# Kernel tuning notes

Measured on AMD Instinct MI355X. Metric: run time of the kernel, lower is better.

The kernel has to match this reference:

```python
import jax, jax.numpy as jnp
import numpy as np

N_NODES = 50000
N_EDGES = 600000
NFEAT = 256
NHID = 128
NCLASS = 40


def setup_inputs() -> dict:
    key = jax.random.key(0)
    ks = jax.random.split(key, 10)
    x = jax.random.normal(ks[0], (N_NODES, NFEAT), dtype=jnp.float32)
    edge_src = jax.random.randint(ks[1], (N_EDGES,), 0, N_NODES, dtype=jnp.int32)
    edge_dst = jax.random.randint(ks[2], (N_EDGES,), 0, N_NODES, dtype=jnp.int32)
    # normalized adjacency weights (positive, ~1/deg scale)
    edge_weight = jax.random.uniform(ks[3], (N_EDGES,), dtype=jnp.float32) * 0.2
    # GraphConvolution params (Glorot-ish init)
    W1 = jax.random.normal(ks[4], (NFEAT, NHID), dtype=jnp.float32) / np.float32(np.sqrt(NFEAT))
    b1 = jnp.zeros((NHID,), dtype=jnp.float32)
    W2 = jax.random.normal(ks[5], (NHID, NHID), dtype=jnp.float32) / np.float32(np.sqrt(NHID))
    b2 = jnp.zeros((NHID,), dtype=jnp.float32)
    W3 = jax.random.normal(ks[6], (NHID, NCLASS), dtype=jnp.float32) / np.float32(np.sqrt(NHID))
    b3 = jnp.zeros((NCLASS,), dtype=jnp.float32)
    return {"x": x, "edge_weight": edge_weight, "W1": W1, "b1": b1,
            "W2": W2, "b2": b2, "W3": W3, "b3": b3,
            "edge_src": edge_src, "edge_dst": edge_dst}


def _gcn_layer(h, W, b, edge_src, edge_dst, edge_weight):
    # support = h @ W ; out = spmm(adj, support) + b
    support = h @ W                                   # [N, out]
    msgs = support[edge_src] * edge_weight[:, None]   # [E, out]
    agg = jax.ops.segment_sum(msgs, edge_dst, num_segments=N_NODES)
    return agg + b


def reference(x, edge_weight, W1, b1, W2, b2, W3, b3, edge_src, edge_dst):
    # eval mode: F.dropout(training=False) is identity
    h = jax.nn.relu(_gcn_layer(x, W1, b1, edge_src, edge_dst, edge_weight))
    h = jax.nn.relu(_gcn_layer(h, W2, b2, edge_src, edge_dst, edge_weight))
    h = _gcn_layer(h, W3, b3, edge_src, edge_dst, edge_weight)
    return jax.nn.log_softmax(h, axis=1)
```

## Files before the change

### kernel.cpp

```cpp
#include <hip/hip_runtime.h>
#include <math.h>

#define N_NODES 50000
#define N_EDGES 600000
#define NFEAT   256
#define NHID    128
#define NCLASS  40
#define NBUCK 196
#define EPB_A 2048
#define BUCK_CAP 4096
#define BUCK_WIN 5888
#define BINA_BLOCKS ((N_EDGES + EPB_A - 1) / EPB_A)
#define CVTW_BLOCKS 224
#define GEMM_BLOCKS ((N_NODES + 63) / 64)

typedef __attribute__((ext_vector_type(8))) short bf16x8;
typedef __attribute__((ext_vector_type(4))) float f32x4;
typedef __attribute__((ext_vector_type(2))) float f32x2;

__device__ inline ushort f2bf(float f) {
    uint u = __float_as_uint(f);
    uint r = (u + 0x7fffu + ((u >> 16) & 1u)) >> 16;
    return (ushort)r;
}

__global__ __launch_bounds__(256) void binA_cvtw(const int* __restrict__ src,
                                                 const int* __restrict__ dst,
                                                 const float* __restrict__ w,
                                                 int* __restrict__ bucket_cnt,
                                                 int2* __restrict__ staging, int E,
                                                 const float* __restrict__ W1,
                                                 const float* __restrict__ W2,
                                                 const float* __restrict__ W3,
                                                 ushort* __restrict__ BT1,
                                                 ushort* __restrict__ BT2,
                                                 ushort* __restrict__ BT3) {
    int tid = threadIdx.x;
    if ((int)blockIdx.x >= BINA_BLOCKS) {
        int idx = ((int)blockIdx.x - BINA_BLOCKS) * 256 + tid;
        if (idx < 32768) {
            int nr = idx >> 8, k = idx & 255;
            BT1[idx] = f2bf(W1[(size_t)k * 128 + nr]);
        } else if (idx < 49152) {
            int t = idx - 32768;
            int nr = t >> 7, k = t & 127;
            BT2[t] = f2bf(W2[(size_t)k * 128 + nr]);
        } else if (idx < 57344) {
            int t = idx - 49152;
            int nr = t >> 7, k = t & 127;
            BT3[t] = (nr < 40) ? f2bf(W3[(size_t)k * 40 + nr]) : (ushort)0;
        }
        return;
    }
    __shared__ int lh[NBUCK];
    for (int b = tid; b < NBUCK; b += 256) lh[b] = 0;
    __syncthreads();
    int base = blockIdx.x * EPB_A;
    int d[8];
    #pragma unroll
    for (int j = 0; j < 8; ++j) {
        int i = base + j * 256 + tid;
        d[j] = (i < E) ? dst[i] : -1;
        if (d[j] >= 0) atomicAdd(&lh[d[j] >> 8], 1);
    }
    __syncthreads();
    for (int b = tid; b < NBUCK; b += 256) {
        int c = lh[b];
        lh[b] = c ? (b * BUCK_CAP + atomicAdd(&bucket_cnt[b], c)) : 0;
    }
    __syncthreads();
    #pragma unroll
    for (int j = 0; j < 8; ++j) {
        int i = base + j * 256 + tid;
        if (d[j] >= 0) {
            int slot = atomicAdd(&lh[d[j] >> 8], 1);
            uint rec = ((uint)f2bf(w[i]) << 16) | (uint)src[i];
            staging[slot] = make_int2((int)rec, d[j] & 255);
        }
    }
}

template<int NT, bool AF32>
__device__ __forceinline__ void gemm_body(const void* __restrict__ Ain,
                                          const ushort* __restrict__ BT,
                                          int M, int K, int Nout,
                                          ushort* __restrict__ Cout, int row0) {
    __shared__ ushort a_s[64 * 40];
    __shared__ ushort b_s[64 * NT * 40];
    int tid = threadIdx.x;
    int wave = tid >> 6, lane = tid & 63;
    int lr = lane & 15, lk = (lane >> 4) * 8;
    f32x4 acc[4][NT];
    #pragma unroll
    for (int mt = 0; mt < 4; ++mt)
        #pragma unroll
        for (int nt = 0; nt < NT; ++nt) acc[mt][nt] = (f32x4){0.f, 0.f, 0.f, 0.f};

    for (int k0 = 0; k0 < K; k0 += 32) {
        {
            int r = tid >> 2, c8 = (tid & 3) * 8;
            int gr = row0 + r; if (gr >= M) gr = M - 1;
            if (AF32) {
                const float* Af = (const float*)Ain;
                float4 v0 = *(const float4*)(Af + (size_t)gr * K + k0 + c8);
                float4 v1 = *(const float4*)(Af + (size_t)gr * K + k0 + c8 + 4);
                ushort4 o0, o1;
                o0.x = f2bf(v0.x); o0.y = f2bf(v0.y); o0.z = f2bf(v0.z); o0.w = f2bf(v0.w);
                o1.x = f2bf(v1.x); o1.y = f2bf(v1.y); o1.z = f2bf(v1.z); o1.w = f2bf(v1.w);
                *(ushort4*)(a_s + r * 40 + c8) = o0;
                *(ushort4*)(a_s + r * 40 + c8 + 4) = o1;
            } else {
                const ushort* Ab = (const ushort*)Ain;
                float4 v = *(const float4*)(Ab + (size_t)gr * K + k0 + c8);
                *(float4*)(a_s + r * 40 + c8) = v;
            }
        }
        #pragma unroll
        for (int i = 0; i < NT; ++i) {
            int idx = tid * NT + i;
            int r = idx >> 2, c8 = (idx & 3) * 8;
            float4 v = *(const float4*)(BT + (size_t)r * K + k0 + c8);
            *(float4*)(b_s + r * 40 + c8) = v;
        }
        __syncthreads();
        bf16x8 bfr[NT];
        #pragma unroll
        for (int nt = 0; nt < NT; ++nt)
            bfr[nt] = *(const bf16x8*)(b_s + ((wave * NT + nt) * 16 + lr) * 40 + lk);
        #pragma unroll
        for (int mt = 0; mt < 4; ++mt) {
            bf16x8 afr = *(const bf16x8*)(a_s + (mt * 16 + lr) * 40 + lk);
            #pragma unroll
            for (int nt = 0; nt < NT; ++nt)
                acc[mt][nt] = __builtin_amdgcn_mfma_f32_16x16x32_bf16(
                    afr, bfr[nt], acc[mt][nt], 0, 0, 0);
        }
        __syncthreads();
    }
    int col0 = wave * NT * 16;
    #pragma unroll
    for (int mt = 0; mt < 4; ++mt) {
        int gr0 = row0 + mt * 16 + (lane >> 4) * 4;
        #pragma unroll
        for (int nt = 0; nt < NT; ++nt) {
            int gc = col0 + nt * 16 + lr;
            #pragma unroll
            for (int i = 0; i < 4; ++i) {
                int gr = gr0 + i;
                if (gr < M && gc < Nout)
                    Cout[(size_t)gr * Nout + gc] = f2bf(acc[mt][nt][i]);
            }
        }
    }
}

__global__ __launch_bounds__(256) void scan_gemm1(const int* __restrict__ bucket_cnt,
                                                  const int2* __restrict__ staging,
                                                  int2* __restrict__ rsp2,
                                                  uint* __restrict__ edges,
                                                  const float* __restrict__ x,
                                                  const ushort* __restrict__ BT1,
                                                  ushort* __restrict__ supA) {
    if ((int)blockIdx.x >= NBUCK) {
        gemm_body<2, true>(x, BT1, N_NODES, 256, 128, supA,
                           ((int)blockIdx.x - NBUCK) * 64);
        return;
    }
    __shared__ int hist[256];
    __shared__ int buf[256];
    __shared__ int lcur[256];
    int tid = threadIdx.x;
    hist[tid] = 0;
    __syncthreads();
    int b = blockIdx.x;
    int c = bucket_cnt[b];
    const int2* st = staging + (size_t)b * BUCK_CAP;
    for (int p = tid; p < c; p += 256) atomicAdd(&hist[st[p].y], 1);
    __syncthreads();
    int v = (hist[tid] + 7) & ~7;
    buf[tid] = v;
    __syncthreads();
    #pragma unroll
    for (int off = 1; off < 256; off <<= 1) {
        int t = (tid >= off) ? buf[tid - off] : 0;
        __syncthreads();
        buf[tid] += t;
        __syncthreads();
    }
    int bb = b * BUCK_WIN;
    int ex = buf[tid] - v + bb;
    int i = b * 256 + tid;
    if (i < N_NODES) rsp2[i] = make_int2(ex, ex + v);
    lcur[tid] = ex;
    __syncthreads();
    int e0 = bb + buf[255];
    for (int p = bb + tid; p < e0; p += 256) edges[p] = 0;
    __syncthreads();
    for (int p = tid; p < c; p += 256) {
        int2 r = st[p];
        int slot = atomicAdd(&lcur[r.y], 1);
        edges[slot] = (uint)r.x;
    }
}


#define LDREC(Ra, Rb, Rc, Rd, POS) do { \
    const uint4* _p = (const uint4*)(edges + (POS)); \
    Ra = _p[0]; Rb = _p[1]; Rc = _p[2]; Rd = _p[3]; \
} while (0)

#define GATHER(P, W, Ra, Rb, Rc, Rd) do { \
    uint _r[16] = {Ra.x, Ra.y, Ra.z, Ra.w, Rb.x, Rb.y, Rb.z, Rb.w, \
                   Rc.x, Rc.y, Rc.z, Rc.w, Rd.x, Rd.y, Rd.z, Rd.w}; \
    _Pragma("unroll") \
    for (int _j = 0; _j < 16; ++_j) { \
        uint _idx = _r[_j] & 0xffffu; \
        if (_idx >= N_NODES) _idx = N_NODES - 1;   \
        P[_j] = sup[(size_t)_idx * 64 + lane]; \
        W[_j] = __uint_as_float(_r[_j] & 0xffff0000u); \
    } \
} while (0)

#define FLUSH1() do { \
    uint _pk = ((uint)f2bf(fmaxf(acc2.y + by, 0.f)) << 16) \
             |  (uint)f2bf(fmaxf(acc2.x + bx, 0.f)); \
    *(uint*)(&a4_s[ks][(wave * 16 + cur) * 40 + kk]) = _pk; \
    acc2 = (f32x2){0.f, 0.f}; \
    ++cur; \
    e_cur = (cur < 16) ? e_s[wave][cur + 1] : 0x7fffffff; \
} while (0)

#define FMA_CHUNK(QB, P, W) do { \
    _Pragma("unroll") \
    for (int _g = 0; _g < 2; ++_g) { \
        int _qg = (QB) + _g * 8; \
        while (cur < 16 && _qg >= e_cur) FLUSH1(); \
        if (_qg < QE) { \
            _Pragma("unroll") \
            for (int _j = 0; _j < 8; ++_j) { \
                uint _pv = P[_g * 8 + _j]; \
                f32x2 _v; \
                _v.x = __uint_as_float(_pv << 16); \
                _v.y = __uint_as_float(_pv & 0xffff0000u); \
                float _w = W[_g * 8 + _j]; \
                acc2 += _v * (f32x2){_w, _w}; \
            } \
        } \
    } \
} while (0)

template<int NT>
__device__ __forceinline__ void fused_body(const uint* __restrict__ sup,
                                           const int2* __restrict__ rsp2,
                                           const uint* __restrict__ edges,
                                           const float* __restrict__ bias,
                                           const ushort* __restrict__ BT,
                                           int Nout,
                                           ushort* __restrict__ Cout) {
    __shared__ ushort a4_s[4][64 * 40];
    __shared__ int e_s[4][17];
    int tid = threadIdx.x;
    int wave = tid >> 6, lane = tid & 63;
    int row0 = blockIdx.x * 64;
    int nfirst = row0 + wave * 16;
    float bx = bias[2 * lane], by = bias[2 * lane + 1];
    int ks = lane >> 4;
    int kk = 2 * (lane & 15);

    if (lane < 16) {
        int nd = nfirst + lane; if (nd >= N_NODES) nd = N_NODES - 1;
        int2 t = rsp2[nd];
        e_s[wave][lane + 1] = t.y;
        if (lane == 0) e_s[wave][0] = t.x;
    }
    __syncthreads();
    int Q = e_s[wave][0], QE = e_s[wave][16];
    int cur = 0, e_cur = e_s[wave][1];
    f32x2 acc2 = (f32x2){0.f, 0.f};

    uint4 rA0, rA1, rA2, rA3, rB0, rB1, rB2, rB3;
    uint pa[16], pb[16];
    float wa[16], wb[16];
    int q = Q;
    LDREC(rA0, rA1, rA2, rA3, q);
    GATHER(pa, wa, rA0, rA1, rA2, rA3);
    LDREC(rB0, rB1, rB2, rB3, q + 16);
    while (q < QE) {
        GATHER(pb, wb, rB0, rB1, rB2, rB3);
        LDREC(rA0, rA1, rA2, rA3, q + 32);
        FMA_CHUNK(q, pa, wa);
        q += 16;
        if (q >= QE) break;
        GATHER(pa, wa, rA0, rA1, rA2, rA3);
        LDREC(rB0, rB1, rB2, rB3, q + 32);
        FMA_CHUNK(q, pb, wb);
        q += 16;
    }
    while (cur < 16) FLUSH1();
    __syncthreads();

    int lr = lane & 15, lk = (lane >> 4) * 8;
    f32x4 acc[4][NT];
    #pragma unroll
    for (int mt = 0; mt < 4; ++mt)
        #pragma unroll
        for (int nt = 0; nt < NT; ++nt) acc[mt][nt] = (f32x4){0.f, 0.f, 0.f, 0.f};
    #pragma unroll
    for (int ksi = 0; ksi < 4; ++ksi) {
        int k0 = ksi * 32;
        bf16x8 bfr[NT];
        #pragma unroll
        for (int nt = 0; nt < NT; ++nt)
            bfr[nt] = *(const bf16x8*)(BT +
                (size_t)((wave * NT + nt) * 16 + lr) * 128 + k0 + lk);
        #pragma unroll
        for (int mt = 0; mt < 4; ++mt) {
            bf16x8 afr = *(const bf16x8*)(&a4_s[ksi][(mt * 16 + lr) * 40 + lk]);
            #pragma unroll
            for (int nt = 0; nt < NT; ++nt)
                acc[mt][nt] = __builtin_amdgcn_mfma_f32_16x16x32_bf16(
                    afr, bfr[nt], acc[mt][nt], 0, 0, 0);
        }
    }
    int col0 = wave * NT * 16;
    #pragma unroll
    for (int mt = 0; mt < 4; ++mt) {
        int gr0 = row0 + mt * 16 + (lane >> 4) * 4;
        #pragma unroll
        for (int nt = 0; nt < NT; ++nt) {
            int gc = col0 + nt * 16 + lr;
            #pragma unroll
            for (int i = 0; i < 4; ++i) {
                int gr = gr0 + i;
                if (gr < N_NODES && gc < Nout)
                    Cout[(size_t)gr * Nout + gc] = f2bf(acc[mt][nt][i]);
            }
        }
    }
}

__global__ __launch_bounds__(256) void fused_ag2(const uint* __restrict__ sup,
                                                 const int2* __restrict__ rsp2,
                                                 const uint* __restrict__ edges,
                                                 const float* __restrict__ bias,
                                                 const ushort* __restrict__ BT,
                                                 ushort* __restrict__ Cout) {
    fused_body<2>(sup, rsp2, edges, bias, BT, 128, Cout);
}

__global__ __launch_bounds__(256) void fused_ag3(const uint* __restrict__ sup,
                                                 const int2* __restrict__ rsp2,
                                                 const uint* __restrict__ edges,
                                                 const float* __restrict__ bias,
                                                 const ushort* __restrict__ BT,
                                                 ushort* __restrict__ Cout) {
    fused_body<1>(sup, rsp2, edges, bias, BT, 40, Cout);
}

__global__ __launch_bounds__(256) void spmm40_lsm(const ushort* __restrict__ sup,
                                                  const int2* __restrict__ rsp2,
                                                  const uint* __restrict__ edges,
                                                  const float* __restrict__ bias,
                                                  float* __restrict__ out, int n) {
    int wid = blockIdx.x * 4 + (threadIdx.x >> 6);
    int lane = threadIdx.x & 63;
    if (wid >= n) return;
    int2 ke = rsp2[wid];
    int k = ke.x, e = ke.y;
    float acc = 0.f;
    int lf = (lane < 40) ? lane : 39;
    if (k < e) {
        const uint4* q4 = (const uint4*)(edges + k);
        uint4 qa = q4[0], qb = q4[1];
        for (; k < e; k += 8) {
            int kn = k + 8;
            int kc = (kn < e) ? kn : k;
            const uint4* n4 = (const uint4*)(edges + kc);
            uint4 na = n4[0], nb4 = n4[1];
            uint q[8] = {qa.x, qa.y, qa.z, qa.w, qb.x, qb.y, qb.z, qb.w};
            float p[8];
            #pragma unroll
            for (int j = 0; j < 8; ++j) {
                uint us = sup[(size_t)(q[j] & 0xffffu) * 40 + lf];
                p[j] = __uint_as_float(us << 16);
            }
            #pragma unroll
            for (int j = 0; j < 8; ++j)
                acc += p[j] * __uint_as_float(q[j] & 0xffff0000u);
            qa = na; qb = nb4;
        }
    }
    float v = (lane < 40) ? acc + bias[lane] : -INFINITY;
    float m = v;
    #pragma unroll
    for (int off = 32; off; off >>= 1) m = fmaxf(m, __shfl_xor(m, off, 64));
    float ex = (lane < 40) ? expf(v - m) : 0.f;
    float s = ex;
    #pragma unroll
    for (int off = 32; off; off >>= 1) s += __shfl_xor(s, off, 64);
    float ls = logf(s);
    if (lane < 40) out[(size_t)wid * 40 + lane] = v - m - ls;
}

extern "C" void kernel_launch(void* const* d_in, const int* in_sizes, int n_in,
                              void* d_out, int out_size, void* d_ws, size_t ws_size,
                              hipStream_t stream) {
    const float* x   = (const float*)d_in[0];
    const float* ew  = (const float*)d_in[1];
    const float* W1  = (const float*)d_in[2];
    const float* b1  = (const float*)d_in[3];
    const float* W2  = (const float*)d_in[4];
    const float* b2  = (const float*)d_in[5];
    const float* W3  = (const float*)d_in[6];
    const float* b3  = (const float*)d_in[7];
    const int* esrc  = (const int*)d_in[8];
    const int* edst  = (const int*)d_in[9];
    float* out = (float*)d_out;

    char* ws = (char*)d_ws;
    size_t off = 0;
    auto alloc = [&](size_t bytes) {
        size_t cur = off;
        off += (bytes + 255) & ~(size_t)255;
        return cur;
    };
    int* bucket_cnt = (int*)(ws + alloc(256 * sizeof(int)));
    int2* rsp2   = (int2*)(ws + alloc((size_t)N_NODES * sizeof(int2)));
    uint* edges  = (uint*)(ws + alloc((size_t)NBUCK * BUCK_WIN * sizeof(uint)));
    int2* staging = (int2*)(ws + alloc((size_t)NBUCK * BUCK_CAP * sizeof(int2)));
    ushort* BT1  = (ushort*)(ws + alloc(128 * 256 * 2));
    ushort* BT2  = (ushort*)(ws + alloc(128 * 128 * 2));
    ushort* BT3  = (ushort*)(ws + alloc(64 * 128 * 2));
    char* Sreg   = ws + alloc((size_t)N_NODES * 128 * 2);
    char* Hreg   = ws + alloc((size_t)N_NODES * 128 * 2);
    (void)alloc((size_t)66000 * 128 * 2);

    ushort* supA = (ushort*)Sreg;
    ushort* supB = (ushort*)Hreg;
    ushort* sup3 = (ushort*)Sreg;

    hipMemsetAsync(bucket_cnt, 0, 256 * sizeof(int), stream);
    binA_cvtw<<<BINA_BLOCKS + CVTW_BLOCKS, 256, 0, stream>>>(
        esrc, edst, ew, bucket_cnt, staging, N_EDGES, W1, W2, W3, BT1, BT2, BT3);
    scan_gemm1<<<NBUCK + GEMM_BLOCKS, 256, 0, stream>>>(
        bucket_cnt, staging, rsp2, edges, x, BT1, supA);
    fused_ag2<<<GEMM_BLOCKS, 256, 0, stream>>>(
        (const uint*)supA, rsp2, edges, b1, BT2, supB);
    fused_ag3<<<GEMM_BLOCKS, 256, 0, stream>>>(
        (const uint*)supB, rsp2, edges, b2, BT3, sup3);
    spmm40_lsm<<<(N_NODES + 3) / 4, 256, 0, stream>>>(sup3, rsp2, edges, b3,
                                                      out, N_NODES);
}
```

Baseline: 216.2 us.

## Halve fused aggregation tile to 32 rows and use segmented final aggregation with log-softmax

The fused aggregate+GEMM kernels now process 32 nodes per block (8 per wave), which doubles the block count and shrinks shared memory. The third-layer support is stored with a 64-column padded stride so the final layer can reuse the prefetched, segmented edge-walk pattern. The old one-wave-per-node spmm40_lsm kernel is replaced by agg_lsm, which streams edges across 8 nodes per wave and runs log-softmax at each node boundary. The trade-offs are more per-block setup and less MFMA reuse per B-fragment load, plus a wider sup3 write with 24 wasted columns.

Result: no change. 215.4 us (-0.4%).

```diff
diff --git a/kernel.cpp b/kernel.cpp
--- a/kernel.cpp
+++ b/kernel.cpp
@@ -13,6 +13,7 @@
 #define BINA_BLOCKS ((N_EDGES + EPB_A - 1) / EPB_A)
 #define CVTW_BLOCKS 224
 #define GEMM_BLOCKS ((N_NODES + 63) / 64)
+#define TILE_BLOCKS ((N_NODES + 31) / 32)
 
 typedef __attribute__((ext_vector_type(8))) short bf16x8;
 typedef __attribute__((ext_vector_type(4))) float f32x4;
@@ -221,20 +222,20 @@
     } \
 } while (0)
 
-#define FLUSH1() do { \
+#define FLUSH_A() do { \
     uint _pk = ((uint)f2bf(fmaxf(acc2.y + by, 0.f)) << 16) \
              |  (uint)f2bf(fmaxf(acc2.x + bx, 0.f)); \
-    *(uint*)(&a4_s[ks][(wave * 16 + cur) * 40 + kk]) = _pk; \
+    *(uint*)(&a4_s[ks][(wave * 8 + cur) * 40 + kk]) = _pk; \
     acc2 = (f32x2){0.f, 0.f}; \
     ++cur; \
-    e_cur = (cur < 16) ? e_s[wave][cur + 1] : 0x7fffffff; \
-} while (0)
-
-#define FMA_CHUNK(QB, P, W) do { \
+    e_cur = (cur < 8) ? e_s[wave][cur + 1] : 0x7fffffff; \
+} while (0)
+
+#define FMA_CHUNK_A(QB, P, W) do { \
     _Pragma("unroll") \
     for (int _g = 0; _g < 2; ++_g) { \
         int _qg = (QB) + _g * 8; \
-        while (cur < 16 && _qg >= e_cur) FLUSH1(); \
+        while (cur < 8 && _qg >= e_cur) FLUSH_A(); \
         if (_qg < QE) { \
             _Pragma("unroll") \
             for (int _j = 0; _j < 8; ++_j) { \
@@ -257,24 +258,24 @@
                                            const ushort* __restrict__ BT,
                                            int Nout,
                                            ushort* __restrict__ Cout) {
-    __shared__ ushort a4_s[4][64 * 40];
-    __shared__ int e_s[4][17];
+    __shared__ ushort a4_s[4][32 * 40];
+    __shared__ int e_s[4][9];
     int tid = threadIdx.x;
     int wave = tid >> 6, lane = tid & 63;
-    int row0 = blockIdx.x * 64;
-    int nfirst = row0 + wave * 16;
+    int row0 = blockIdx.x * 32;
+    int nfirst = row0 + wave * 8;
     float bx = bias[2 * lane], by = bias[2 * lane + 1];
     int ks = lane >> 4;
     int kk = 2 * (lane & 15);
 
-    if (lane < 16) {
+    if (lane < 8) {
         int nd = nfirst + lane; if (nd >= N_NODES) nd = N_NODES - 1;
         int2 t = rsp2[nd];
         e_s[wave][lane + 1] = t.y;
         if (lane == 0) e_s[wave][0] = t.x;
     }
     __syncthreads();
-    int Q = e_s[wave][0], QE = e_s[wave][16];
+    int Q = e_s[wave][0], QE = e_s[wave][8];
     int cur = 0, e_cur = e_s[wave][1];
     f32x2 acc2 = (f32x2){0.f, 0.f};
 
@@ -288,21 +289,21 @@
     while (q < QE) {
         GATHER(pb, wb, rB0, rB1, rB2, rB3);
         LDREC(rA0, rA1, rA2, rA3, q + 32);
-        FMA_CHUNK(q, pa, wa);
+        FMA_CHUNK_A(q, pa, wa);
         q += 16;
         if (q >= QE) break;
         GATHER(pa, wa, rA0, rA1, rA2, rA3);
         LDREC(rB0, rB1, rB2, rB3, q + 32);
-        FMA_CHUNK(q, pb, wb);
+        FMA_CHUNK_A(q, pb, wb);
         q += 16;
     }
-    while (cur < 16) FLUSH1();
+    while (cur < 8) FLUSH_A();
     __syncthreads();
 
     int lr = lane & 15, lk = (lane >> 4) * 8;
-    f32x4 acc[4][NT];
-    #pragma unroll
-    for (int mt = 0; mt < 4; ++mt)
+    f32x4 acc[2][NT];
+    #pragma unroll
+    for (int mt = 0; mt < 2; ++mt)
         #pragma unroll
         for (int nt = 0; nt < NT; ++nt) acc[mt][nt] = (f32x4){0.f, 0.f, 0.f, 0.f};
     #pragma unroll
@@ -314,7 +315,7 @@
             bfr[nt] = *(const bf16x8*)(BT +
                 (size_t)((wave * NT + nt) * 16 + lr) * 128 + k0 + lk);
         #pragma unroll
-        for (int mt = 0; mt < 4; ++mt) {
+        for (int mt = 0; mt < 2; ++mt) {
             bf16x8 afr = *(const bf16x8*)(&a4_s[ksi][(mt * 16 + lr) * 40 + lk]);
             #pragma unroll
             for (int nt = 0; nt < NT; ++nt)
@@ -324,7 +325,7 @@
     }
     int col0 = wave * NT * 16;
     #pragma unroll
-    for (int mt = 0; mt < 4; ++mt) {
+    for (int mt = 0; mt < 2; ++mt) {
         int gr0 = row0 + mt * 16 + (lane >> 4) * 4;
         #pragma unroll
         for (int nt = 0; nt < NT; ++nt) {
@@ -354,52 +355,93 @@
                                                  const float* __restrict__ bias,
                                                  const ushort* __restrict__ BT,
                                                  ushort* __restrict__ Cout) {
-    fused_body<1>(sup, rsp2, edges, bias, BT, 40, Cout);
-}
-
-__global__ __launch_bounds__(256) void spmm40_lsm(const ushort* __restrict__ sup,
-                                                  const int2* __restrict__ rsp2,
-                                                  const uint* __restrict__ edges,
-                                                  const float* __restrict__ bias,
-                                                  float* __restrict__ out, int n) {
-    int wid = blockIdx.x * 4 + (threadIdx.x >> 6);
-    int lane = threadIdx.x & 63;
-    if (wid >= n) return;
-    int2 ke = rsp2[wid];
-    int k = ke.x, e = ke.y;
-    float acc = 0.f;
-    int lf = (lane < 40) ? lane : 39;
-    if (k < e) {
-        const uint4* q4 = (const uint4*)(edges + k);
-        uint4 qa = q4[0], qb = q4[1];
-        for (; k < e; k += 8) {
-            int kn = k + 8;
-            int kc = (kn < e) ? kn : k;
-            const uint4* n4 = (const uint4*)(edges + kc);
-            uint4 na = n4[0], nb4 = n4[1];
-            uint q[8] = {qa.x, qa.y, qa.z, qa.w, qb.x, qb.y, qb.z, qb.w};
-            float p[8];
-            #pragma unroll
-            for (int j = 0; j < 8; ++j) {
-                uint us = sup[(size_t)(q[j] & 0xffffu) * 40 + lf];
-                p[j] = __uint_as_float(us << 16);
-            }
-            #pragma unroll
-            for (int j = 0; j < 8; ++j)
-                acc += p[j] * __uint_as_float(q[j] & 0xffff0000u);
-            qa = na; qb = nb4;
-        }
-    }
-    float v = (lane < 40) ? acc + bias[lane] : -INFINITY;
-    float m = v;
-    #pragma unroll
-    for (int off = 32; off; off >>= 1) m = fmaxf(m, __shfl_xor(m, off, 64));
-    float ex = (lane < 40) ? expf(v - m) : 0.f;
-    float s = ex;
-    #pragma unroll
-    for (int off = 32; off; off >>= 1) s += __shfl_xor(s, off, 64);
-    float ls = logf(s);
-    if (lane < 40) out[(size_t)wid * 40 + lane] = v - m - ls;
+    fused_body<1>(sup, rsp2, edges, bias, BT, 64, Cout);
+}
+
+
+#define GATHER_U16(P, W, Ra, Rb, Rc, Rd) do { \
+    uint _r[16] = {Ra.x, Ra.y, Ra.z, Ra.w, Rb.x, Rb.y, Rb.z, Rb.w, \
+                   Rc.x, Rc.y, Rc.z, Rc.w, Rd.x, Rd.y, Rd.z, Rd.w}; \
+    _Pragma("unroll") \
+    for (int _j = 0; _j < 16; ++_j) { \
+        uint _idx = _r[_j] & 0xffffu; \
+        if (_idx >= N_NODES) _idx = N_NODES - 1; \
+        P[_j] = __uint_as_float((uint)sup[(size_t)_idx * 64 + lane] << 16); \
+        W[_j] = __uint_as_float(_r[_j] & 0xffff0000u); \
+    } \
+} while (0)
+
+#define FLUSH_L() do { \
+    int _node = nfirst + cur; \
+    float _v = (lane < 40) ? acc1 + bl : -INFINITY; \
+    float _m = _v; \
+    _Pragma("unroll") \
+    for (int _o = 32; _o; _o >>= 1) _m = fmaxf(_m, __shfl_xor(_m, _o, 64)); \
+    float _ex = (lane < 40) ? expf(_v - _m) : 0.f; \
+    float _s = _ex; \
+    _Pragma("unroll") \
+    for (int _o = 32; _o; _o >>= 1) _s += __shfl_xor(_s, _o, 64); \
+    float _ls = logf(_s); \
+    if (lane < 40 && _node < N_NODES) \
+        out[(size_t)_node * 40 + lane] = _v - _m - _ls; \
+    acc1 = 0.f; \
+    ++cur; \
+    e_cur = (cur < 8) ? e_s[wave][cur + 1] : 0x7fffffff; \
+} while (0)
+
+#define FMA_CHUNK_L(QB, P, W) do { \
+    _Pragma("unroll") \
+    for (int _g = 0; _g < 2; ++_g) { \
+        int _qg = (QB) + _g * 8; \
+        while (cur < 8 && _qg >= e_cur) FLUSH_L(); \
+        if (_qg < QE) { \
+            _Pragma("unroll") \
+            for (int _j = 0; _j < 8; ++_j) \
+                acc1 += P[_g * 8 + _j] * W[_g * 8 + _j]; \
+        } \
+    } \
+} while (0)
+
+__global__ __launch_bounds__(256) void agg_lsm(const ushort* __restrict__ sup,
+                                               const int2* __restrict__ rsp2,
+                                               const uint* __restrict__ edges,
+                                               const float* __restrict__ bias,
+                                               float* __restrict__ out) {
+    __shared__ int e_s[4][9];
+    int tid = threadIdx.x;
+    int wave = tid >> 6, lane = tid & 63;
+    int nfirst = blockIdx.x * 32 + wave * 8;
+    float bl = (lane < 40) ? bias[lane] : 0.f;
+    if (lane < 8) {
+        int nd = nfirst + lane; if (nd >= N_NODES) nd = N_NODES - 1;
+        int2 t = rsp2[nd];
+        e_s[wave][lane + 1] = t.y;
+        if (lane == 0) e_s[wave][0] = t.x;
+    }
+    __syncthreads();
+    int Q = e_s[wave][0], QE = e_s[wave][8];
+    int cur = 0, e_cur = e_s[wave][1];
+    float acc1 = 0.f;
+
+    uint4 rA0, rA1, rA2, rA3, rB0, rB1, rB2, rB3;
+    float pa[16], pb[16];
+    float wa[16], wb[16];
+    int q = Q;
+    LDREC(rA0, rA1, rA2, rA3, q);
+    GATHER_U16(pa, wa, rA0, rA1, rA2, rA3);
+    LDREC(rB0, rB1, rB2, rB3, q + 16);
+    while (q < QE) {
+        GATHER_U16(pb, wb, rB0, rB1, rB2, rB3);
+        LDREC(rA0, rA1, rA2, rA3, q + 32);
+        FMA_CHUNK_L(q, pa, wa);
+        q += 16;
+        if (q >= QE) break;
+        GATHER_U16(pa, wa, rA0, rA1, rA2, rA3);
+        LDREC(rB0, rB1, rB2, rB3, q + 32);
+        FMA_CHUNK_L(q, pb, wb);
+        q += 16;
+    }
+    while (cur < 8) FLUSH_L();
 }
 
 extern "C" void kernel_launch(void* const* d_in, const int* in_sizes, int n_in,
@@ -444,10 +486,9 @@
         esrc, edst, ew, bucket_cnt, staging, N_EDGES, W1, W2, W3, BT1, BT2, BT3);
     scan_gemm1<<<NBUCK + GEMM_BLOCKS, 256, 0, stream>>>(
         bucket_cnt, staging, rsp2, edges, x, BT1, supA);
-    fused_ag2<<<GEMM_BLOCKS, 256, 0, stream>>>(
+    fused_ag2<<<TILE_BLOCKS, 256, 0, stream>>>(
         (const uint*)supA, rsp2, edges, b1, BT2, supB);
-    fused_ag3<<<GEMM_BLOCKS, 256, 0, stream>>>(
+    fused_ag3<<<TILE_BLOCKS, 256, 0, stream>>>(
         (const uint*)supB, rsp2, edges, b2, BT3, sup3);
-    spmm40_lsm<<<(N_NODES + 3) / 4, 256, 0, stream>>>(sup3, rsp2, edges, b3,
-                                                      out, N_NODES);
-}
+    agg_lsm<<<TILE_BLOCKS, 256, 0, stream>>>(sup3, rsp2, edges, b3, out);
+}
```
